# Optimization experiments

Measured on AMD Instinct MI355X. Metric: run time of the kernel, lower is better.

Reference implementation:

```python
import jax, jax.numpy as jnp
import numpy as np

K = 7            # neighbor volumes (NNN heads)
PS = 10          # patch size
ADJ = PS // 2    # patch anchor offset (use_adj)
WOFF = 29 // 2   # search window half-size (ws=29)
KSEARCH = 224    # hardcoded in forward
T, C, E, HH, WW = 1, 8, 8, 64, 64


def _box1(a, axis):
    # sliding-window sum of length PS anchored at i-ADJ, zero outside
    pw = [(0, 0)] * a.ndim
    pw[axis] = (ADJ, PS - 1 - ADJ)
    ap = jnp.pad(a, pw)
    c = jnp.cumsum(ap, axis=axis)
    zp = [(0, 0)] * a.ndim
    zp[axis] = (1, 0)
    c = jnp.pad(c, zp)
    n = a.shape[axis]
    return jax.lax.slice_in_dim(c, PS, PS + n, axis=axis) - jax.lax.slice_in_dim(c, 0, n, axis=axis)


def box_sum(a):
    return _box1(_box1(a, -2), -1)


def setup_inputs():
    key = jax.random.key(0)
    ks = jax.random.split(key, 5)
    x = jax.random.normal(ks[0], (T, C, HH, WW), jnp.float32)
    xe = jax.random.normal(ks[1], (T, E, HH, WW), jnp.float32)
    ye = jax.random.normal(ks[2], (T, E, HH, WW), jnp.float32)
    y = jax.random.normal(ks[3], (T, C, HH, WW), jnp.float32)
    log_temp = 0.1 * jax.random.normal(ks[4], (T, 1, HH, WW), jnp.float32)
    return {"x": x, "xe": xe, "ye": ye, "y": y, "log_temp": log_temp}


def reference(x, xe, ye, y, log_temp):
    pad = lambda a: jnp.pad(a, ((0, 0), (0, 0), (1, 1), (1, 1)))
    x, xe, ye, y, log_temp = pad(x), pad(xe), pad(ye), pad(y), pad(log_temp)
    H, W = x.shape[-2:]
    Q = H * W
    xe0, ye0 = xe[0], ye[0]
    # search window offsets (ws x ws)
    dy, dx = np.meshgrid(np.arange(-WOFF, WOFF + 1), np.arange(-WOFF, WOFF + 1), indexing='ij')
    dy = jnp.asarray(dy.ravel()); dx = jnp.asarray(dx.ravel())
    nW = dy.shape[0]  # 841
    # patch squared norms (zero padded patches)
    n2_q = box_sum((ye0 ** 2).sum(0))   # (H,W)
    n2_db = box_sum((xe0 ** 2).sum(0))  # (H,W)
    xep = jnp.pad(xe0, ((0, 0), (WOFF, WOFF), (WOFF, WOFF)))
    n2p = jnp.pad(n2_db, WOFF)
    def shifted(d):
        s = jax.lax.dynamic_slice(xep, (0, WOFF + d[0], WOFF + d[1]), (E, H, W))
        n = jax.lax.dynamic_slice(n2p, (WOFF + d[0], WOFF + d[1]), (H, W))
        return s, n
    xe_s, n2_s = jax.vmap(shifted)(jnp.stack([dy, dx], -1))  # (nW,E,H,W),(nW,H,W)
    cross = box_sum((ye0[None] * xe_s).sum(1))               # (nW,H,W)
    dist = n2_q[None] + n2_s - 2.0 * cross                   # L2^2, (nW,H,W)
    qy = jnp.arange(H)[:, None]; qx = jnp.arange(W)[None, :]
    valid = ((qy[None] + dy[:, None, None] >= 0) & (qy[None] + dy[:, None, None] < H)
             & (qx[None] + dx[:, None, None] >= 0) & (qx[None] + dx[:, None, None] < W))
    self_m = (dy == 0) & (dx == 0)  # remove_self
    dist = jnp.where(valid & ~self_m[:, None, None], dist, 1e10)
    dist = dist.transpose(1, 2, 0).reshape(Q, nW)
    negd, idx = jax.lax.top_k(-dist, KSEARCH)  # closest KSEARCH, negd = -L2
    # avg-pooled log temperature per query patch
    lt = (box_sum(log_temp[0, 0]) / (PS * PS)).reshape(Q)
    # NeuralNearestNeighbors: iterative continuous top-k relaxation
    logits = negd / jnp.exp(lt)[:, None]
    Ws = []
    for _ in range(K):
        w = jax.nn.softmax(logits, axis=-1)
        logits = logits + jnp.log(jnp.clip(1.0 - w, 1e-6, None))
        Ws.append(w)
    Wk = jnp.stack(Ws)  # (K,Q,KSEARCH)
    # absolute candidate coords
    qyf = jnp.repeat(jnp.arange(H), W); qxf = jnp.tile(jnp.arange(W), H)
    ny = qyf[:, None] + dy[idx]; nx = qxf[:, None] + dx[idx]  # (Q,KSEARCH)
    # weighted patch sum (gather per patch offset)
    xpad = jnp.pad(x[0], ((0, 0), (ADJ, PS - 1 - ADJ), (ADJ, PS - 1 - ADJ)))
    z = jnp.zeros((K, Q, C, PS, PS), x.dtype)
    for oy in range(PS):
        for ox in range(PS):
            vals = xpad[:, ny + oy, nx + ox]  # (C,Q,KSEARCH)
            z = z.at[:, :, :, oy, ox].set(jnp.einsum('kqj,cqj->kqc', Wk, vals))
    # fold with counting (iFoldz): overlap-add of patches + coverage counts
    zp = z.transpose(1, 0, 2, 3, 4).reshape(H, W, K * C, PS, PS)
    buf = jnp.zeros((K * C, H + PS - 1, W + PS - 1), x.dtype)
    cnt = jnp.zeros((H + PS - 1, W + PS - 1), x.dtype)
    for oy in range(PS):
        for ox in range(PS):
            buf = buf.at[:, oy:oy + H, ox:ox + W].add(zp[:, :, :, oy, ox].transpose(2, 0, 1))
            cnt = cnt.at[oy:oy + H, ox:ox + W].add(1.0)
    vid = buf[:, ADJ:ADJ + H, ADJ:ADJ + W]
    zvid = cnt[ADJ:ADJ + H, ADJ:ADJ + W]
    zagg = vid / zvid[None]
    zagg = zagg.reshape(T, K, C, H, W) - y.reshape(T, 1, C, H, W)
    zagg = zagg.reshape(T, K * C, H, W)
    out = jnp.concatenate([y, zagg], axis=1)[..., 1:-1, 1:-1]
    return out
```

## Files before the change

kernel.cpp:

```cpp
#include <hip/hip_runtime.h>
#include <hip/hip_bf16.h>

#define HP    66
#define QTOT  (HP*HP)
#define LSTR  67
#define NWIN  29
#define NW    (NWIN*NWIN)
#define KK    7
#define WOFF2 14
#define NZ    15
#define QB    8
#define QBN   545
#define NIT   27
#define NSEG3 198


__global__ __launch_bounds__(256) void k_prep1(const float* __restrict__ x,
    const float* __restrict__ xe, const float* __restrict__ ye,
    const float* __restrict__ lt, float* __restrict__ ws) {
  int p = blockIdx.x * 256 + threadIdx.x;
  if (p >= QTOT) return;
  int i = p / HP, j = p % HP;
  bool in = (i >= 1 && i < HP-1 && j >= 1 && j < HP-1);
  int src = (i-1)*64 + (j-1);
  float* ye66 = ws;
  float* xe66 = ws + 8*QTOT;
  float* x66p = ws + 16*QTOT;
  float sy = 0.f, sx = 0.f;
#pragma unroll
  for (int e = 0; e < 8; ++e) {
    float vy = in ? ye[e*4096 + src] : 0.f;
    float vx = in ? xe[e*4096 + src] : 0.f;
    float vv = in ? x [e*4096 + src] : 0.f;
    ye66[e*QTOT + p] = vy;
    xe66[e*QTOT + p] = vx;
    x66p[e*QTOT + p] = vv;
    sy += vy*vy; sx += vx*vx;
  }
  ws[24*QTOT + p] = sy;
  ws[25*QTOT + p] = sx;
  ws[26*QTOT + p] = in ? lt[src] : 0.f;
}

__global__ __launch_bounds__(256) void k_prep2(float* __restrict__ ws) {
  int p = blockIdx.x * 256 + threadIdx.x;
  if (p >= QTOT) return;
  int i = p / HP, j = p % HP;
  const float* sqye = ws + 24*QTOT;
  const float* sqxe = ws + 25*QTOT;
  const float* lt66 = ws + 26*QTOT;
  float a = 0.f, b = 0.f, c = 0.f;
  for (int u = -5; u <= 4; ++u) {
    int ii = i + u; if (ii < 0 || ii >= HP) continue;
    for (int v = -5; v <= 4; ++v) {
      int jj = j + v; if (jj < 0 || jj >= HP) continue;
      int o = ii*HP + jj;
      a += sqye[o]; b += sqxe[o]; c += lt66[o];
    }
  }
  ws[27*QTOT + p] = a;
  ws[28*QTOT + p] = b;
  ws[29*QTOT + p] = c * 0.01f;
}

__global__ __launch_bounds__(256) void k_dist(const float* __restrict__ ws,
                                              float* __restrict__ dist) {
  __shared__ float s[HP*LSTR];
  __shared__ float h[HP*LSTR];
  int w = blockIdx.x, tid = threadIdx.x;
  int dy = w / NWIN - WOFF2, dx = w % NWIN - WOFF2;
  const float* ye66 = ws;
  const float* xe66 = ws + 8*QTOT;
  const float* n2q  = ws + 27*QTOT;
  const float* n2db = ws + 28*QTOT;
  for (int p = tid; p < QTOT; p += 256) {
    int i = p / HP, j = p % HP;
    int ii = i + dy, jj = j + dx;
    float sv = 0.f;
    if (ii >= 0 && ii < HP && jj >= 0 && jj < HP) {
      int p2 = ii*HP + jj;
#pragma unroll
      for (int e = 0; e < 8; ++e) sv += ye66[e*QTOT + p] * xe66[e*QTOT + p2];
    }
    s[i*LSTR + j] = sv;
  }
  __syncthreads();
  if (tid < NSEG3) {
    int row = tid % HP, seg = tid / HP, c0 = seg*22;
    const float* ar = s + row*LSTR;
    float* hr = h + row*LSTR;
    float w9[9]; float sum = 0.f;
#pragma unroll
    for (int t = 0; t < 9; ++t) {
      int jj = c0 - 5 + t;
      float v = (jj >= 0) ? ar[jj] : 0.f;
      w9[t] = v; sum += v;
    }
#pragma unroll
    for (int t = 0; t < 22; ++t) {
      int j = c0 + t, jn = j + 4;
      float nv = (jn < HP) ? ar[jn] : 0.f;
      sum += nv;
      hr[j] = sum;
      sum -= w9[t % 9];
      w9[t % 9] = nv;
    }
  }
  __syncthreads();
  if (tid < NSEG3) {
    int col = tid % HP, seg = tid / HP, r0 = seg*22;
    float w9[9]; float sum = 0.f;
#pragma unroll
    for (int t = 0; t < 9; ++t) {
      int ii = r0 - 5 + t;
      float v = (ii >= 0) ? h[ii*LSTR + col] : 0.f;
      w9[t] = v; sum += v;
    }
#pragma unroll
    for (int t = 0; t < 22; ++t) {
      int i = r0 + t, in2 = i + 4;
      float nv = (in2 < HP) ? h[in2*LSTR + col] : 0.f;
      sum += nv;
      float cr = sum;
      int p = i*HP + col;
      int ii = i + dy, jj = col + dx;
      bool valid = (ii >= 0 && ii < HP && jj >= 0 && jj < HP);
      float dv = 1e10f;
      if (valid && !(dy == 0 && dx == 0))
        dv = n2q[p] + n2db[ii*HP + jj] - 2.f * cr;
      dist[w*QTOT + p] = dv;
      sum -= w9[t % 9];
      w9[t % 9] = nv;
    }
  }
}

__global__ __launch_bounds__(256) void k_weights(const float* __restrict__ ws,
    const float* __restrict__ dist, __hip_bfloat16* __restrict__ wf) {
  __shared__ float mh[32], sh[32];
  int tid = threadIdx.x;
  int qq = tid & (QB-1);
  int qb = blockIdx.x;
  int q = qb * QB + qq;
  bool qok = q < QTOT;
  int qs = qok ? q : (QTOT - 1);
  int wg = tid >> 3;
  int wave = tid >> 6;
  float invT = __expf(-ws[29*QTOT + qs]);
  float lv[NIT], ev[NIT];
#pragma unroll
  for (int it = 0; it < NIT; ++it) {
    int w = wg + it*32;
    lv[it] = (qok && w < NW) ? (-dist[w*QTOT + qs] * invT) : -3.0e38f;
  }
  for (int k = 0; k < KK; ++k) {
    float pm = -3.0e38f;
#pragma unroll
    for (int it = 0; it < NIT; ++it) pm = fmaxf(pm, lv[it]);
    pm = fmaxf(pm, __shfl_xor(pm, 8, 64));
    pm = fmaxf(pm, __shfl_xor(pm, 16, 64));
    pm = fmaxf(pm, __shfl_xor(pm, 32, 64));
    if ((tid & 63) < QB) mh[wave*QB + qq] = pm;
    __syncthreads();
    float m = fmaxf(fmaxf(mh[qq], mh[QB+qq]), fmaxf(mh[2*QB+qq], mh[3*QB+qq]));
    float psum = 0.f;
#pragma unroll
    for (int it = 0; it < NIT; ++it) {
      float e = __expf(lv[it] - m);
      ev[it] = e;
      psum += e;
    }
    psum += __shfl_xor(psum, 8, 64);
    psum += __shfl_xor(psum, 16, 64);
    psum += __shfl_xor(psum, 32, 64);
    if ((tid & 63) < QB) sh[wave*QB + qq] = psum;
    __syncthreads();
    float invden = 1.0f / (sh[qq] + sh[QB+qq] + sh[2*QB+qq] + sh[3*QB+qq]);
    size_t bkq = ((size_t)k*QBN + qb)*NW;
#pragma unroll
    for (int it = 0; it < NIT; ++it) {
      int w = wg + it*32;
      if (qok && w < NW) {
        float wgt = ev[it] * invden;
        wf[(bkq + w)*8 + qq] = __float2bfloat16(wgt);
        if (k < KK-1 && wgt > 1e-9f)
          lv[it] += __logf(fmaxf(1.f - wgt, 1e-6f));
      }
    }
    __syncthreads();
  }
}

__global__ __launch_bounds__(256) void k_boxw(__hip_bfloat16* __restrict__ wfp) {
  __shared__ uint4 au4[546];
  __shared__ float h[QTOT];
  int bid = blockIdx.x;
  int l = (bid & 7)*736 + (bid >> 3);
  if (l >= KK*NW) return;
  int k = l / NW, w = l % NW;
  uint4* u4 = (uint4*)wfp;
  size_t pb = ((size_t)k*QBN)*NW + w;
  int tid = threadIdx.x;
  for (int qb = tid; qb < QBN; qb += 256)
    au4[qb] = u4[pb + (size_t)qb*NW];
  if (tid < 8) ((unsigned short*)au4)[4356 + tid] = 0;
  __syncthreads();
  const unsigned short* a16 = (const unsigned short*)au4;
  if (tid < NSEG3) {
    int row = tid % HP, seg = tid / HP, c0 = seg*22;
    const unsigned short* ar = a16 + row*HP;
    float* hr = h + row*HP;
    float w9[9]; float sum = 0.f;
#pragma unroll
    for (int t = 0; t < 9; ++t) {
      int jj = c0 - 4 + t;
      float v = (jj >= 0) ? __uint_as_float((unsigned)ar[jj] << 16) : 0.f;
      w9[t] = v; sum += v;
    }
#pragma unroll
    for (int t = 0; t < 22; ++t) {
      int j = c0 + t, jn = j + 5;
      float nv = (jn < HP) ? __uint_as_float((unsigned)ar[jn] << 16) : 0.f;
      sum += nv;
      hr[j] = sum;
      sum -= w9[t % 9];
      w9[t % 9] = nv;
    }
  }
  __syncthreads();
  unsigned short* a16w = (unsigned short*)au4;
  if (tid < NSEG3) {
    int col = tid % HP, seg = tid / HP, r0 = seg*22;
    float w9[9]; float sum = 0.f;
#pragma unroll
    for (int t = 0; t < 9; ++t) {
      int ii = r0 - 4 + t;
      float v = (ii >= 0) ? h[ii*HP + col] : 0.f;
      w9[t] = v; sum += v;
    }
#pragma unroll
    for (int t = 0; t < 22; ++t) {
      int i = r0 + t, in2 = i + 5;
      float nv = (in2 < HP) ? h[in2*HP + col] : 0.f;
      sum += nv;
      a16w[i*HP + col] = __bfloat16_as_ushort(__float2bfloat16(sum));
      sum -= w9[t % 9];
      w9[t % 9] = nv;
    }
  }
  __syncthreads();
  for (int qb = tid; qb < QBN; qb += 256)
    u4[pb + (size_t)qb*NW] = au4[qb];
}

__global__ __launch_bounds__(256) void k_contract(const float* __restrict__ ws,
    const unsigned short* __restrict__ wfu, float* __restrict__ accb2) {
  __shared__ float xt[8][17][45];
  int t = blockIdx.x, z = blockIdx.y, k = blockIdx.z, tid = threadIdx.x;
  int I0 = (t >> 2) * 16, J0 = (t & 3) * 16;
  int dylo = -WOFF2 + 2*z;
  int gy0 = I0 + 1 + dylo, gx0 = J0 - 13;
  const float* x66p = ws + 16*QTOT;
  for (int idx = tid; idx < 8*17*44; idx += 256) {
    int c = idx / (17*44);
    int rem = idx % (17*44);
    int r = rem / 44, cc = rem % 44;
    int gy = gy0 + r, gx = gx0 + cc;
    float v = 0.f;
    if (gy >= 0 && gy < HP && gx >= 0 && gx < HP) v = x66p[c*QTOT + gy*HP + gx];
    xt[c][r][cc] = v;
  }
  __syncthreads();
  int il = tid >> 4, jl = tid & 15;
  int I = I0 + 1 + il, J = J0 + 1 + jl;
  int pix = I*HP + J;
  int qb = pix >> 3, q7 = pix & 7;
  size_t cb = (((size_t)k*QBN + qb)*NW)*8 + q7;
  float acc[8];
#pragma unroll
  for (int c = 0; c < 8; ++c) acc[c] = 0.f;
  int ndd = (z == NZ-1) ? 1 : 2;
  for (int dd = 0; dd < ndd; ++dd) {
    int wrow = (dylo + dd + WOFF2) * NWIN;
    const unsigned short* wp = wfu + cb + (size_t)wrow*8;
    unsigned short wv[NWIN];
#pragma unroll
    for (int dxw = 0; dxw < NWIN; ++dxw) wv[dxw] = wp[dxw*8];
#pragma unroll
    for (int dxw = 0; dxw < NWIN; ++dxw) {
      float wgt = __uint_as_float((unsigned)wv[dxw] << 16);
      int r = il + dd, col = jl + dxw;
#pragma unroll
      for (int c = 0; c < 8; ++c) acc[c] += wgt * xt[c][r][col];
    }
  }
  int px64 = (I-1)*64 + (J-1);
#pragma unroll
  for (int c = 0; c < 8; ++c)
    accb2[((z*56 + k*8 + c)*4096) + px64] = acc[c];
}

__global__ __launch_bounds__(256) void k_final(const float* __restrict__ y,
    const float* __restrict__ accb2, float* __restrict__ out) {
  int idx = blockIdx.x * 256 + threadIdx.x;
  int ch = idx >> 12, px = idx & 4095;
  if (ch < 8) { out[idx] = y[ch*4096 + px]; return; }
  int kc = ch - 8, c = kc & 7;
  int i = px >> 6, j = px & 63;
  int I = i + 1, J = j + 1;
  int cy = min(I+5, HP-1) - max(I-4, 0) + 1;
  int cx = min(J+5, HP-1) - max(J-4, 0) + 1;
  float s = 0.f;
  for (int z = 0; z < NZ; ++z) s += accb2[(z*56 + kc)*4096 + px];
  out[idx] = s / (float)(cy*cx) - y[c*4096 + px];
}

extern "C" void kernel_launch(void* const* d_in, const int* in_sizes, int n_in,
                              void* d_out, int out_size, void* d_ws, size_t ws_size,
                              hipStream_t stream) {
  const float* x  = (const float*)d_in[0];
  const float* xe = (const float*)d_in[1];
  const float* ye = (const float*)d_in[2];
  const float* y  = (const float*)d_in[3];
  const float* lt = (const float*)d_in[4];
  float* ws   = (float*)d_ws;
  float* dist = ws + 30*QTOT;
  __hip_bfloat16* wf = (__hip_bfloat16*)(dist + (size_t)NW*QTOT);
  float* accb2 = dist;
  float* out = (float*)d_out;

  k_prep1<<<(QTOT + 255)/256, 256, 0, stream>>>(x, xe, ye, lt, ws);
  k_prep2<<<(QTOT + 255)/256, 256, 0, stream>>>(ws);
  k_dist<<<NW, 256, 0, stream>>>(ws, dist);
  k_weights<<<QBN, 256, 0, stream>>>(ws, dist, wf);
  k_boxw<<<KK*NW, 256, 0, stream>>>(wf);
  k_contract<<<dim3(16, NZ, KK), 256, 0, stream>>>(ws, (const unsigned short*)wf, accb2);
  k_final<<<out_size/256, 256, 0, stream>>>(y, accb2, out);
}
```

Baseline: 158.6 us.

## Store padded embeddings channel-interleaved and use float4 loads in dist and contract

```diff
diff --git a/kernel.cpp b/kernel.cpp
--- a/kernel.cpp
+++ b/kernel.cpp
@@ -23,20 +23,24 @@
   int i = p / HP, j = p % HP;
   bool in = (i >= 1 && i < HP-1 && j >= 1 && j < HP-1);
   int src = (i-1)*64 + (j-1);
-  float* ye66 = ws;
-  float* xe66 = ws + 8*QTOT;
-  float* x66p = ws + 16*QTOT;
+  float vy[8], vx[8], vv[8];
   float sy = 0.f, sx = 0.f;
 #pragma unroll
   for (int e = 0; e < 8; ++e) {
-    float vy = in ? ye[e*4096 + src] : 0.f;
-    float vx = in ? xe[e*4096 + src] : 0.f;
-    float vv = in ? x [e*4096 + src] : 0.f;
-    ye66[e*QTOT + p] = vy;
-    xe66[e*QTOT + p] = vx;
-    x66p[e*QTOT + p] = vv;
-    sy += vy*vy; sx += vx*vx;
-  }
+    vy[e] = in ? ye[e*4096 + src] : 0.f;
+    vx[e] = in ? xe[e*4096 + src] : 0.f;
+    vv[e] = in ? x [e*4096 + src] : 0.f;
+    sy += vy[e]*vy[e]; sx += vx[e]*vx[e];
+  }
+  float4* yp = (float4*)(ws + (size_t)p*8);
+  float4* xp = (float4*)(ws + 8*QTOT + (size_t)p*8);
+  float4* vp = (float4*)(ws + 16*QTOT + (size_t)p*8);
+  yp[0] = make_float4(vy[0], vy[1], vy[2], vy[3]);
+  yp[1] = make_float4(vy[4], vy[5], vy[6], vy[7]);
+  xp[0] = make_float4(vx[0], vx[1], vx[2], vx[3]);
+  xp[1] = make_float4(vx[4], vx[5], vx[6], vx[7]);
+  vp[0] = make_float4(vv[0], vv[1], vv[2], vv[3]);
+  vp[1] = make_float4(vv[4], vv[5], vv[6], vv[7]);
   ws[24*QTOT + p] = sy;
   ws[25*QTOT + p] = sx;
   ws[26*QTOT + p] = in ? lt[src] : 0.f;
@@ -69,8 +73,8 @@
   __shared__ float h[HP*LSTR];
   int w = blockIdx.x, tid = threadIdx.x;
   int dy = w / NWIN - WOFF2, dx = w % NWIN - WOFF2;
-  const float* ye66 = ws;
-  const float* xe66 = ws + 8*QTOT;
+  const float* yex = ws;
+  const float* xex = ws + 8*QTOT;
   const float* n2q  = ws + 27*QTOT;
   const float* n2db = ws + 28*QTOT;
   for (int p = tid; p < QTOT; p += 256) {
@@ -79,8 +83,11 @@
     float sv = 0.f;
     if (ii >= 0 && ii < HP && jj >= 0 && jj < HP) {
       int p2 = ii*HP + jj;
-#pragma unroll
-      for (int e = 0; e < 8; ++e) sv += ye66[e*QTOT + p] * xe66[e*QTOT + p2];
+      const float4* yp = (const float4*)(yex + (size_t)p*8);
+      const float4* xp = (const float4*)(xex + (size_t)p2*8);
+      float4 a0 = yp[0], a1 = yp[1], b0 = xp[0], b1 = xp[1];
+      sv += a0.x*b0.x; sv += a0.y*b0.y; sv += a0.z*b0.z; sv += a0.w*b0.w;
+      sv += a1.x*b1.x; sv += a1.y*b1.y; sv += a1.z*b1.z; sv += a1.w*b1.w;
     }
     s[i*LSTR + j] = sv;
   }
@@ -147,7 +154,7 @@
   int wg = tid >> 3;
   int wave = tid >> 6;
   float invT = __expf(-ws[29*QTOT + qs]);
-  float lv[NIT], ev[NIT];
+  float lv[NIT];
 #pragma unroll
   for (int it = 0; it < NIT; ++it) {
     int w = wg + it*32;
@@ -165,11 +172,7 @@
     float m = fmaxf(fmaxf(mh[qq], mh[QB+qq]), fmaxf(mh[2*QB+qq], mh[3*QB+qq]));
     float psum = 0.f;
 #pragma unroll
-    for (int it = 0; it < NIT; ++it) {
-      float e = __expf(lv[it] - m);
-      ev[it] = e;
-      psum += e;
-    }
+    for (int it = 0; it < NIT; ++it) psum += __expf(lv[it] - m);
     psum += __shfl_xor(psum, 8, 64);
     psum += __shfl_xor(psum, 16, 64);
     psum += __shfl_xor(psum, 32, 64);
@@ -181,7 +184,7 @@
     for (int it = 0; it < NIT; ++it) {
       int w = wg + it*32;
       if (qok && w < NW) {
-        float wgt = ev[it] * invden;
+        float wgt = __expf(lv[it] - m) * invden;
         wf[(bkq + w)*8 + qq] = __float2bfloat16(wgt);
         if (k < KK-1 && wgt > 1e-9f)
           lv[it] += __logf(fmaxf(1.f - wgt, 1e-6f));
@@ -255,20 +258,22 @@
 
 __global__ __launch_bounds__(256) void k_contract(const float* __restrict__ ws,
     const unsigned short* __restrict__ wfu, float* __restrict__ accb2) {
-  __shared__ float xt[8][17][45];
+  __shared__ float xt[17][44][8];
   int t = blockIdx.x, z = blockIdx.y, k = blockIdx.z, tid = threadIdx.x;
   int I0 = (t >> 2) * 16, J0 = (t & 3) * 16;
   int dylo = -WOFF2 + 2*z;
   int gy0 = I0 + 1 + dylo, gx0 = J0 - 13;
-  const float* x66p = ws + 16*QTOT;
-  for (int idx = tid; idx < 8*17*44; idx += 256) {
-    int c = idx / (17*44);
-    int rem = idx % (17*44);
-    int r = rem / 44, cc = rem % 44;
+  const float* x66i = ws + 16*QTOT;
+  for (int idx = tid; idx < 17*44; idx += 256) {
+    int r = idx / 44, cc = idx % 44;
     int gy = gy0 + r, gx = gx0 + cc;
-    float v = 0.f;
-    if (gy >= 0 && gy < HP && gx >= 0 && gx < HP) v = x66p[c*QTOT + gy*HP + gx];
-    xt[c][r][cc] = v;
+    float4 v0 = make_float4(0.f,0.f,0.f,0.f), v1 = v0;
+    if (gy >= 0 && gy < HP && gx >= 0 && gx < HP) {
+      const float4* xp = (const float4*)(x66i + (size_t)(gy*HP + gx)*8);
+      v0 = xp[0]; v1 = xp[1];
+    }
+    float4* d = (float4*)&xt[r][cc][0];
+    d[0] = v0; d[1] = v1;
   }
   __syncthreads();
   int il = tid >> 4, jl = tid & 15;
@@ -286,12 +291,16 @@
     unsigned short wv[NWIN];
 #pragma unroll
     for (int dxw = 0; dxw < NWIN; ++dxw) wv[dxw] = wp[dxw*8];
+    int r = il + dd;
 #pragma unroll
     for (int dxw = 0; dxw < NWIN; ++dxw) {
       float wgt = __uint_as_float((unsigned)wv[dxw] << 16);
-      int r = il + dd, col = jl + dxw;
-#pragma unroll
-      for (int c = 0; c < 8; ++c) acc[c] += wgt * xt[c][r][col];
+      const float4* xr = (const float4*)&xt[r][jl + dxw][0];
+      float4 x0 = xr[0], x1 = xr[1];
+      acc[0] += wgt * x0.x; acc[1] += wgt * x0.y;
+      acc[2] += wgt * x0.z; acc[3] += wgt * x0.w;
+      acc[4] += wgt * x1.x; acc[5] += wgt * x1.y;
+      acc[6] += wgt * x1.z; acc[7] += wgt * x1.w;
     }
   }
   int px64 = (I-1)*64 + (J-1);
```

Result: faster. 145.9 us (-8.0%).
